# Optimization experiments

Measured on AMD Instinct MI355X. Metric: run time of the kernel, lower is better.

The kernel has to match this reference:

```python
import jax, jax.numpy as jnp
import numpy as np
import math

B, S, H, DK = 16, 4096, 16, 64
DM = H * DK          # 1024, d_model
QD = 1024            # q_d_model
KVD = 1024           # kv_d_model
MASK_P = 0.85        # randbool probability


def setup_inputs() -> dict:
    key = jax.random.key(0)
    ks = jax.random.split(key, 12)
    s = 0.02
    return {
        "q": jax.random.normal(ks[0], (B, 1, QD), jnp.float32),
        "k": jax.random.normal(ks[1], (B, S, KVD), jnp.float32),
        "v": jax.random.normal(ks[2], (B, S, KVD), jnp.float32),
        "Wq": jax.random.normal(ks[3], (QD, DM), jnp.float32) * s,
        "bq": jnp.zeros((DM,), jnp.float32),
        "Wk": jax.random.normal(ks[4], (KVD, DM), jnp.float32) * s,
        "bk": jnp.zeros((DM,), jnp.float32),
        "Wv": jax.random.normal(ks[5], (KVD, DM), jnp.float32) * s,
        "bv": jnp.zeros((DM,), jnp.float32),
        "Wo": jax.random.normal(ks[6], (DM, QD), jnp.float32) * s,
        "bo": jnp.zeros((QD,), jnp.float32),
        # randbool(shape, p=0.85): True where rand < p -> score zeroed
        "maskfill": jax.random.uniform(ks[7], (B, H, 1, S)) < MASK_P,
    }


def reference(q, k, v, Wq, bq, Wk, bk, Wv, bv, Wo, bo, maskfill):
    bs = q.shape[0]
    # projections -> [B, L, H, DK] -> [B, H, L, DK]
    qh = (q @ Wq + bq).reshape(bs, -1, H, DK).transpose(0, 2, 1, 3)  # [B,H,1,DK]
    kh = (k @ Wk + bk).reshape(bs, -1, H, DK).transpose(0, 2, 1, 3)  # [B,H,S,DK]
    vh = (v @ Wv + bv).reshape(bs, -1, H, DK).transpose(0, 2, 1, 3)  # [B,H,S,DK]

    scores1 = jnp.einsum("bhqd,bhkd->bhqk", qh, kh) / math.sqrt(DK)  # [B,H,1,S]

    # plain path (dropout = identity in eval)
    attn = jax.nn.softmax(scores1, axis=-1)
    out_h = jnp.einsum("bhqk,bhkd->bhqd", attn, vh)                  # [B,H,1,DK]

    # masked path: zero-fill (not -inf) masked raw scores, then softmax
    masked_scores = jnp.where(maskfill, 0.0, scores1)
    mattn = jax.nn.softmax(masked_scores, axis=-1)
    mout_h = jnp.einsum("bhqk,bhkd->bhqd", mattn, vh)

    concat = out_h.transpose(0, 2, 1, 3).reshape(bs, DM)
    mconcat = mout_h.transpose(0, 2, 1, 3).reshape(bs, DM)
    output = concat @ Wo + bo
    masked_output = mconcat @ Wo + bo
    return (output, masked_output)
```

## Files before the change

kernel.cpp:

```cpp
#include <hip/hip_runtime.h>
#include <stdint.h>

#define NB 16
#define NS 4096
#define NH 16
#define NC 1024

#define OFF_QHP   0u
#define OFF_QK    262144u
#define OFF_QB    524288u
#define OFF_FLAG  524544u
#define OFF_SP    524608u
#define OFF_S     532800u
#define OFF_ATT   533312u
#define OFF_CTXP  2630464u
#define OFF_CTX   6824768u
#define OFF_CON   7349056u

__global__ void k_maskprobe(const uint32_t* __restrict__ m, int* __restrict__ flag) {
    __shared__ int sf, sg;
    if (threadIdx.x == 0) { sf = 0; sg = 0; }
    __syncthreads();
    uint32_t x = m[threadIdx.x];
    if (x == 0x3F800000u) atomicOr(&sf, 1);
    else if (x > 1u) atomicOr(&sg, 1);
    __syncthreads();
    if (threadIdx.x == 0) *flag = sf ? 2 : (sg ? 1 : 0);
}

__global__ __launch_bounds__(128) void k_qh(
    const float* __restrict__ q, const float* __restrict__ Wq, float* __restrict__ qhp)
{
    __shared__ float qs[64*16];
    int dz = blockIdx.x, cs = blockIdx.y;
    int tid = threadIdx.x;
    int d = dz*128 + tid;
#pragma unroll
    for (int j = 0; j < 2; ++j) {
        int idx = j*128 + tid;
        int b = idx >> 4, c4 = (idx & 15) << 2;
        float4 t = *(const float4*)(q + (size_t)b*NC + cs*64 + c4);
        qs[(c4+0)*16 + b] = t.x; qs[(c4+1)*16 + b] = t.y;
        qs[(c4+2)*16 + b] = t.z; qs[(c4+3)*16 + b] = t.w;
    }
    __syncthreads();
    float acc[16];
#pragma unroll
    for (int b = 0; b < 16; ++b) acc[b] = 0.f;
#pragma unroll 4
    for (int c = 0; c < 64; ++c) {
        float w = Wq[(size_t)(cs*64 + c)*NC + d];
        const float4* qr = (const float4*)(qs + c*16);
        float4 q0 = qr[0], q1 = qr[1], q2 = qr[2], q3 = qr[3];
        acc[0]  = fmaf(w, q0.x, acc[0]);  acc[1]  = fmaf(w, q0.y, acc[1]);
        acc[2]  = fmaf(w, q0.z, acc[2]);  acc[3]  = fmaf(w, q0.w, acc[3]);
        acc[4]  = fmaf(w, q1.x, acc[4]);  acc[5]  = fmaf(w, q1.y, acc[5]);
        acc[6]  = fmaf(w, q1.z, acc[6]);  acc[7]  = fmaf(w, q1.w, acc[7]);
        acc[8]  = fmaf(w, q2.x, acc[8]);  acc[9]  = fmaf(w, q2.y, acc[9]);
        acc[10] = fmaf(w, q2.z, acc[10]); acc[11] = fmaf(w, q2.w, acc[11]);
        acc[12] = fmaf(w, q3.x, acc[12]); acc[13] = fmaf(w, q3.y, acc[13]);
        acc[14] = fmaf(w, q3.z, acc[14]); acc[15] = fmaf(w, q3.w, acc[15]);
    }
#pragma unroll
    for (int b = 0; b < 16; ++b) qhp[((size_t)cs*16 + b)*NC + d] = acc[b];
}

__global__ __launch_bounds__(128) void k_qk(
    const float* __restrict__ qhp, const float* __restrict__ bq,
    const float* __restrict__ Wk, const float* __restrict__ bk,
    float* __restrict__ qko, float* __restrict__ qbv)
{
    int h = blockIdx.x;
    int c = blockIdx.y*128 + threadIdx.x;
    __shared__ float qs[16*64];
    for (int j = 0; j < 8; ++j) {
        int idx = j*128 + threadIdx.x;
        int b = idx >> 6, dd = idx & 63;
        float a = bq[h*64 + dd];
#pragma unroll
        for (int cs = 0; cs < 16; ++cs) a += qhp[((size_t)cs*16 + b)*NC + h*64 + dd];
        qs[idx] = a;
    }
    __syncthreads();
    const float* wr = Wk + (size_t)c*NC + h*64;
    float acc[16];
#pragma unroll
    for (int b = 0; b < 16; ++b) acc[b] = 0.f;
#pragma unroll 4
    for (int d = 0; d < 64; ++d) {
        float w = wr[d];
#pragma unroll
        for (int b = 0; b < 16; ++b) acc[b] = fmaf(qs[b*64 + d], w, acc[b]);
    }
#pragma unroll
    for (int b = 0; b < 16; ++b) qko[((size_t)b*NH + h)*NC + c] = acc[b];
    if (blockIdx.y == 0 && threadIdx.x < 16) {
        int b = threadIdx.x; float a = 0.f;
        for (int d = 0; d < 64; ++d) a = fmaf(qs[b*64 + d], bk[h*64 + d], a);
        qbv[b*NH + h] = a;
    }
}

#define QTS 20
__global__ __launch_bounds__(256) void k_scoresG(
    const float* __restrict__ kk, const float* __restrict__ qkm,
    const float* __restrict__ qbv, const void* __restrict__ mask,
    const int* __restrict__ flagp, float* __restrict__ att, float* __restrict__ Sp)
{
    __shared__ float qt[NC*QTS];
    __shared__ float red[4][32];
    int sb = blockIdx.x, b = blockIdx.y;
    int tid = threadIdx.x;
    for (int idx = tid; idx < NH*NC; idx += 256) {
        int c = idx & 1023, h = idx >> 10;
        qt[c*QTS + h] = qkm[((size_t)b*NH + h)*NC + c];
    }
    __syncthreads();

    int g = tid >> 2, ph = tid & 3;
    int s0 = sb*256;
    const float* kbase = kk + ((size_t)b*NS + s0 + g*4)*NC + ph*4;
    float acc[4][16];
#pragma unroll
    for (int i = 0; i < 4; ++i)
#pragma unroll
        for (int h = 0; h < 16; ++h) acc[i][h] = 0.f;

    float4 kv[4], kn[4];
#pragma unroll
    for (int i = 0; i < 4; ++i) kv[i] = *(const float4*)(kbase + i*NC);
    for (int w = 0; w < 64; ++w) {
        if (w < 63) {
#pragma unroll
            for (int i = 0; i < 4; ++i)
                kn[i] = *(const float4*)(kbase + i*NC + (w+1)*16);
        }
#pragma unroll
        for (int j = 0; j < 4; ++j) {
            int c = w*16 + ph*4 + j;
            const float* qp = qt + c*QTS;
            float4 q0 = *(const float4*)(qp + 0);
            float4 q1 = *(const float4*)(qp + 4);
            float4 q2 = *(const float4*)(qp + 8);
            float4 q3 = *(const float4*)(qp + 12);
#pragma unroll
            for (int i = 0; i < 4; ++i) {
                float kc = (j == 0) ? kv[i].x : (j == 1) ? kv[i].y
                         : (j == 2) ? kv[i].z : kv[i].w;
                acc[i][0]  = fmaf(kc, q0.x, acc[i][0]);
                acc[i][1]  = fmaf(kc, q0.y, acc[i][1]);
                acc[i][2]  = fmaf(kc, q0.z, acc[i][2]);
                acc[i][3]  = fmaf(kc, q0.w, acc[i][3]);
                acc[i][4]  = fmaf(kc, q1.x, acc[i][4]);
                acc[i][5]  = fmaf(kc, q1.y, acc[i][5]);
                acc[i][6]  = fmaf(kc, q1.z, acc[i][6]);
                acc[i][7]  = fmaf(kc, q1.w, acc[i][7]);
                acc[i][8]  = fmaf(kc, q2.x, acc[i][8]);
                acc[i][9]  = fmaf(kc, q2.y, acc[i][9]);
                acc[i][10] = fmaf(kc, q2.z, acc[i][10]);
                acc[i][11] = fmaf(kc, q2.w, acc[i][11]);
                acc[i][12] = fmaf(kc, q3.x, acc[i][12]);
                acc[i][13] = fmaf(kc, q3.y, acc[i][13]);
                acc[i][14] = fmaf(kc, q3.z, acc[i][14]);
                acc[i][15] = fmaf(kc, q3.w, acc[i][15]);
            }
        }
#pragma unroll
        for (int i = 0; i < 4; ++i) kv[i] = kn[i];
    }

#pragma unroll
    for (int i = 0; i < 4; ++i)
#pragma unroll
        for (int h = 0; h < 16; ++h) {
            acc[i][h] += __shfl_xor(acc[i][h], 1, 64);
            acc[i][h] += __shfl_xor(acc[i][h], 2, 64);
        }

    float sc[16];
#pragma unroll
    for (int i = 0; i < 4; ++i)
        if (ph == i) {
#pragma unroll
            for (int h = 0; h < 16; ++h) sc[h] = acc[i][h];
        }

    int s = s0 + tid;
    int fl = *flagp;
    unsigned mbits = 0;
    if (fl == 1) {
        const uint8_t* mp = (const uint8_t*)mask + (size_t)b*NH*NS + s;
#pragma unroll
        for (int h = 0; h < 16; ++h) if (mp[(size_t)h*NS]) mbits |= (1u << h);
    } else if (fl == 2) {
        const float* mp = (const float*)mask + (size_t)b*NH*NS + s;
#pragma unroll
        for (int h = 0; h < 16; ++h) if (mp[(size_t)h*NS] != 0.f) mbits |= (1u << h);
    } else {
        const int* mp = (const int*)mask + (size_t)b*NH*NS + s;
#pragma unroll
        for (int h = 0; h < 16; ++h) if (mp[(size_t)h*NS]) mbits |= (1u << h);
    }

    float p0[16], p1[16];
    float r0[16], r1[16];
#pragma unroll
    for (int h = 0; h < 16; ++h) {
        float val = (sc[h] + qbv[b*NH + h]) * 0.125f;
        p0[h] = __expf(val);
        p1[h] = (mbits >> h & 1u) ? 1.0f : p0[h];
        r0[h] = p0[h]; r1[h] = p1[h];
    }
    float* arow = att + ((size_t)b*NS + s)*32;
    *(float4*)(arow +  0) = make_float4(p0[0],  p0[1],  p0[2],  p0[3]);
    *(float4*)(arow +  4) = make_float4(p0[4],  p0[5],  p0[6],  p0[7]);
    *(float4*)(arow +  8) = make_float4(p0[8],  p0[9],  p0[10], p0[11]);
    *(float4*)(arow + 12) = make_float4(p0[12], p0[13], p0[14], p0[15]);
    *(float4*)(arow + 16) = make_float4(p1[0],  p1[1],  p1[2],  p1[3]);
    *(float4*)(arow + 20) = make_float4(p1[4],  p1[5],  p1[6],  p1[7]);
    *(float4*)(arow + 24) = make_float4(p1[8],  p1[9],  p1[10], p1[11]);
    *(float4*)(arow + 28) = make_float4(p1[12], p1[13], p1[14], p1[15]);

#pragma unroll
    for (int off = 1; off < 64; off <<= 1)
#pragma unroll
        for (int h = 0; h < 16; ++h) {
            r0[h] += __shfl_xor(r0[h], off, 64);
            r1[h] += __shfl_xor(r1[h], off, 64);
        }
    int wv = tid >> 6;
    if ((tid & 63) == 0) {
#pragma unroll
        for (int h = 0; h < 16; ++h) { red[wv][h] = r0[h]; red[wv][16+h] = r1[h]; }
    }
    __syncthreads();
    if (tid < 32)
        Sp[((size_t)b*16 + sb)*32 + tid] =
            red[0][tid] + red[1][tid] + red[2][tid] + red[3][tid];
}

__global__ void k_sred(const float* __restrict__ Sp, float* __restrict__ S) {
    int t = blockIdx.x*256 + threadIdx.x;
    int p = t >> 8, b = (t >> 4) & 15, h = t & 15;
    float a = 0.f;
#pragma unroll
    for (int sb = 0; sb < 16; ++sb) a += Sp[((size_t)b*16 + sb)*32 + p*16 + h];
    S[t] = a;
}

__global__ __launch_bounds__(256,2) void k_ctx(
    const float* __restrict__ v, const float* __restrict__ att, float* __restrict__ ctxp)
{
    __shared__ float al[64*32];
    __shared__ float buf[8192];
    int b = blockIdx.x & 15, ss = blockIdx.x >> 4;
    int cz = blockIdx.y;
    int tid = threadIdx.x, ct = tid & 63, rg = tid >> 6;
    int s1 = ss * 512;
    float acc[32][4];
#pragma unroll
    for (int i = 0; i < 32; ++i)
#pragma unroll
        for (int j = 0; j < 4; ++j) acc[i][j] = 0.f;

    for (int c0 = 0; c0 < 512; c0 += 64) {
        __syncthreads();
#pragma unroll
        for (int jj = 0; jj < 2; ++jj) {
            int idx = jj*256 + tid;
            ((float4*)al)[idx] = ((const float4*)(att + ((size_t)b*NS + s1 + c0)*32))[idx];
        }
        __syncthreads();
        for (int it = 0; it < 16; ++it) {
            int rl = c0 + it*4 + rg;
            float4 vv = *(const float4*)(v + ((size_t)b*NS + s1 + rl)*NC + cz*256 + ct*4);
            const float4* ar = (const float4*)(al + (it*4 + rg)*32);
#pragma unroll
            for (int u = 0; u < 8; ++u) {
                float4 aw = ar[u];
                acc[u*4+0][0] = fmaf(aw.x, vv.x, acc[u*4+0][0]);
                acc[u*4+0][1] = fmaf(aw.x, vv.y, acc[u*4+0][1]);
                acc[u*4+0][2] = fmaf(aw.x, vv.z, acc[u*4+0][2]);
                acc[u*4+0][3] = fmaf(aw.x, vv.w, acc[u*4+0][3]);
                acc[u*4+1][0] = fmaf(aw.y, vv.x, acc[u*4+1][0]);
                acc[u*4+1][1] = fmaf(aw.y, vv.y, acc[u*4+1][1]);
                acc[u*4+1][2] = fmaf(aw.y, vv.z, acc[u*4+1][2]);
                acc[u*4+1][3] = fmaf(aw.y, vv.w, acc[u*4+1][3]);
                acc[u*4+2][0] = fmaf(aw.z, vv.x, acc[u*4+2][0]);
                acc[u*4+2][1] = fmaf(aw.z, vv.y, acc[u*4+2][1]);
                acc[u*4+2][2] = fmaf(aw.z, vv.z, acc[u*4+2][2]);
                acc[u*4+2][3] = fmaf(aw.z, vv.w, acc[u*4+2][3]);
                acc[u*4+3][0] = fmaf(aw.w, vv.x, acc[u*4+3][0]);
                acc[u*4+3][1] = fmaf(aw.w, vv.y, acc[u*4+3][1]);
                acc[u*4+3][2] = fmaf(aw.w, vv.z, acc[u*4+3][2]);
                acc[u*4+3][3] = fmaf(aw.w, vv.w, acc[u*4+3][3]);
            }
        }
    }
    for (int pr = 0; pr < 4; ++pr) {
        __syncthreads();
#pragma unroll
        for (int u = 0; u < 8; ++u) {
            int ph = pr*8 + u;
            float4 t; t.x = acc[ph][0]; t.y = acc[ph][1]; t.z = acc[ph][2]; t.w = acc[ph][3];
            ((float4*)buf)[(rg*8 + u)*64 + ct] = t;
        }
        __syncthreads();
#pragma unroll
        for (int kx = 0; kx < 2; ++kx) {
            int i = kx*256 + tid;
            int u2 = i >> 6, c2 = i & 63;
            float4 s = ((float4*)buf)[(size_t)(0*8 + u2)*64 + c2];
#pragma unroll
            for (int r2 = 1; r2 < 4; ++r2) {
                float4 t = ((float4*)buf)[(size_t)(r2*8 + u2)*64 + c2];
                s.x += t.x; s.y += t.y; s.z += t.z; s.w += t.w;
            }
            int ph = pr*8 + u2, p = ph >> 4, h = ph & 15;
            *(float4*)(ctxp + ((((size_t)ss*2 + p)*NB + b)*NH + h)*NC + cz*256 + c2*4) = s;
        }
    }
}

__global__ void k_ctxred(const float* __restrict__ ctxp, const float* __restrict__ S,
                         float* __restrict__ ctx) {
    size_t i = (size_t)blockIdx.x * 256 + threadIdx.x;
    float a = 0.f;
#pragma unroll
    for (int ss = 0; ss < 8; ++ss) a += ctxp[(size_t)ss*524288 + i];
    ctx[i] = a / S[i >> 10];
}

__global__ __launch_bounds__(256) void k_outh(
    const float* __restrict__ ctx, const float* __restrict__ Wv,
    const float* __restrict__ bv, float* __restrict__ con)
{
    int b = blockIdx.y, p = blockIdx.z;
    int d = blockIdx.x*256 + threadIdx.x;
    int h0 = blockIdx.x*4;
    __shared__ float cl[4*NC];
    for (int i = threadIdx.x; i < 4*NC; i += 256)
        cl[i] = ctx[(((size_t)p*NB + b)*NH + h0 + (i >> 10))*NC + (i & 1023)];
    __syncthreads();
    const float* c2 = cl + ((threadIdx.x >> 6) << 10);
    float a0=0.f,a1=0.f,a2=0.f,a3=0.f;
    for (int c = 0; c < NC; c += 4) {
        a0 = fmaf(c2[c+0], Wv[(size_t)(c+0)*NC + d], a0);
        a1 = fmaf(c2[c+1], Wv[(size_t)(c+1)*NC + d], a1);
        a2 = fmaf(c2[c+2], Wv[(size_t)(c+2)*NC + d], a2);
        a3 = fmaf(c2[c+3], Wv[(size_t)(c+3)*NC + d], a3);
    }
    con[((size_t)p*NB + b)*NC + d] = (a0+a1)+(a2+a3) + bv[d];
}

__global__ __launch_bounds__(256) void k_out(
    const float* __restrict__ con, const float* __restrict__ Wo,
    const float* __restrict__ bo, float* __restrict__ out)
{
    int b = blockIdx.y, p = blockIdx.z;
    int o = blockIdx.x*256 + threadIdx.x;
    __shared__ float cl[NC];
    for (int i = threadIdx.x; i < NC; i += 256)
        cl[i] = con[((size_t)p*NB + b)*NC + i];
    __syncthreads();
    float a0=0.f,a1=0.f,a2=0.f,a3=0.f;
    for (int m = 0; m < NC; m += 4) {
        a0 = fmaf(cl[m+0], Wo[(size_t)(m+0)*NC + o], a0);
        a1 = fmaf(cl[m+1], Wo[(size_t)(m+1)*NC + o], a1);
        a2 = fmaf(cl[m+2], Wo[(size_t)(m+2)*NC + o], a2);
        a3 = fmaf(cl[m+3], Wo[(size_t)(m+3)*NC + o], a3);
    }
    out[(size_t)p*NB*NC + (size_t)b*NC + o] = (a0+a1)+(a2+a3) + bo[o];
}

extern "C" void kernel_launch(void* const* d_in, const int* in_sizes, int n_in,
                              void* d_out, int out_size, void* d_ws, size_t ws_size,
                              hipStream_t stream)
{
    (void)in_sizes; (void)n_in; (void)out_size; (void)ws_size;
    const float* q  = (const float*)d_in[0];
    const float* k  = (const float*)d_in[1];
    const float* v  = (const float*)d_in[2];
    const float* Wq = (const float*)d_in[3];
    const float* bq = (const float*)d_in[4];
    const float* Wk = (const float*)d_in[5];
    const float* bk = (const float*)d_in[6];
    const float* Wv = (const float*)d_in[7];
    const float* bv = (const float*)d_in[8];
    const float* Wo = (const float*)d_in[9];
    const float* bo = (const float*)d_in[10];
    const void*  mk = d_in[11];

    float* ws   = (float*)d_ws;
    float* qhp  = ws + OFF_QHP;
    float* qkv  = ws + OFF_QK;
    float* qbv  = ws + OFF_QB;
    int*   flg  = (int*)(ws + OFF_FLAG);
    float* Sp   = ws + OFF_SP;
    float* S    = ws + OFF_S;
    float* att  = ws + OFF_ATT;
    float* ctxp = ws + OFF_CTXP;
    float* ctx  = ws + OFF_CTX;
    float* con  = ws + OFF_CON;
    float* out  = (float*)d_out;

    k_maskprobe<<<1, 1024, 0, stream>>>((const uint32_t*)mk, flg);
    k_qh<<<dim3(8, 16), 128, 0, stream>>>(q, Wq, qhp);
    k_qk<<<dim3(16, 8), 128, 0, stream>>>(qhp, bq, Wk, bk, qkv, qbv);
    k_scoresG<<<dim3(16, 16), 256, 0, stream>>>(k, qkv, qbv, mk, flg, att, Sp);
    k_sred<<<2, 256, 0, stream>>>(Sp, S);
    k_ctx<<<dim3(128, 4), 256, 0, stream>>>(v, att, ctxp);
    k_ctxred<<<2048, 256, 0, stream>>>(ctxp, S, ctx);
    k_outh<<<dim3(4, NB, 2), 256, 0, stream>>>(ctx, Wv, bv, con);
    k_out<<<dim3(4, NB, 2), 256, 0, stream>>>(con, Wo, bo, out);
}
```

Baseline: 306.4 us.

## Split scores and context kernels across more blocks for higher occupancy

The scores kernel now gives each block 64 sequence rows instead of 256, so each thread owns one row quarter with 16 accumulators rather than 64. The query-key table is staged through shared memory in four 256-channel chunks, which shrinks the LDS footprint. The grid grows from 256 to 1024 blocks, and the context kernel doubles its grid by halving the span each block covers. The aim is to fill the GPU's compute units better on these two memory-bound passes, at the cost of more partial sums to reduce, more workspace and extra barriers.

```diff
diff --git a/kernel.cpp b/kernel.cpp
--- a/kernel.cpp
+++ b/kernel.cpp
@@ -11,11 +11,11 @@
 #define OFF_QB    524288u
 #define OFF_FLAG  524544u
 #define OFF_SP    524608u
-#define OFF_S     532800u
-#define OFF_ATT   533312u
-#define OFF_CTXP  2630464u
-#define OFF_CTX   6824768u
-#define OFF_CON   7349056u
+#define OFF_S     557376u
+#define OFF_ATT   557888u
+#define OFF_CTXP  2655040u
+#define OFF_CTX   11043648u
+#define OFF_CON   11567936u
 
 __global__ void k_maskprobe(const uint32_t* __restrict__ m, int* __restrict__ flag) {
     __shared__ int sf, sg;
@@ -102,141 +102,116 @@
 }
 
 #define QTS 20
-__global__ __launch_bounds__(256) void k_scoresG(
+__global__ __launch_bounds__(256) void k_scoresG2(
     const float* __restrict__ kk, const float* __restrict__ qkm,
     const float* __restrict__ qbv, const void* __restrict__ mask,
     const int* __restrict__ flagp, float* __restrict__ att, float* __restrict__ Sp)
 {
-    __shared__ float qt[NC*QTS];
-    __shared__ float red[4][32];
+    __shared__ float qt[256*QTS];
+    __shared__ float red[4][2][16];
     int sb = blockIdx.x, b = blockIdx.y;
     int tid = threadIdx.x;
-    for (int idx = tid; idx < NH*NC; idx += 256) {
-        int c = idx & 1023, h = idx >> 10;
-        qt[c*QTS + h] = qkm[((size_t)b*NH + h)*NC + c];
-    }
-    __syncthreads();
-
     int g = tid >> 2, ph = tid & 3;
-    int s0 = sb*256;
-    const float* kbase = kk + ((size_t)b*NS + s0 + g*4)*NC + ph*4;
-    float acc[4][16];
-#pragma unroll
-    for (int i = 0; i < 4; ++i)
-#pragma unroll
-        for (int h = 0; h < 16; ++h) acc[i][h] = 0.f;
-
-    float4 kv[4], kn[4];
-#pragma unroll
-    for (int i = 0; i < 4; ++i) kv[i] = *(const float4*)(kbase + i*NC);
-    for (int w = 0; w < 64; ++w) {
-        if (w < 63) {
-#pragma unroll
-            for (int i = 0; i < 4; ++i)
-                kn[i] = *(const float4*)(kbase + i*NC + (w+1)*16);
-        }
-#pragma unroll
-        for (int j = 0; j < 4; ++j) {
-            int c = w*16 + ph*4 + j;
-            const float* qp = qt + c*QTS;
-            float4 q0 = *(const float4*)(qp + 0);
-            float4 q1 = *(const float4*)(qp + 4);
-            float4 q2 = *(const float4*)(qp + 8);
-            float4 q3 = *(const float4*)(qp + 12);
-#pragma unroll
-            for (int i = 0; i < 4; ++i) {
-                float kc = (j == 0) ? kv[i].x : (j == 1) ? kv[i].y
-                         : (j == 2) ? kv[i].z : kv[i].w;
-                acc[i][0]  = fmaf(kc, q0.x, acc[i][0]);
-                acc[i][1]  = fmaf(kc, q0.y, acc[i][1]);
-                acc[i][2]  = fmaf(kc, q0.z, acc[i][2]);
-                acc[i][3]  = fmaf(kc, q0.w, acc[i][3]);
-                acc[i][4]  = fmaf(kc, q1.x, acc[i][4]);
-                acc[i][5]  = fmaf(kc, q1.y, acc[i][5]);
-                acc[i][6]  = fmaf(kc, q1.z, acc[i][6]);
-                acc[i][7]  = fmaf(kc, q1.w, acc[i][7]);
-                acc[i][8]  = fmaf(kc, q2.x, acc[i][8]);
-                acc[i][9]  = fmaf(kc, q2.y, acc[i][9]);
-                acc[i][10] = fmaf(kc, q2.z, acc[i][10]);
-                acc[i][11] = fmaf(kc, q2.w, acc[i][11]);
-                acc[i][12] = fmaf(kc, q3.x, acc[i][12]);
-                acc[i][13] = fmaf(kc, q3.y, acc[i][13]);
-                acc[i][14] = fmaf(kc, q3.z, acc[i][14]);
-                acc[i][15] = fmaf(kc, q3.w, acc[i][15]);
+    int s = sb*64 + g;
+    const float* kbase = kk + ((size_t)b*NS + s)*NC + ph*4;
+    float acc[16];
+#pragma unroll
+    for (int h = 0; h < 16; ++h) acc[h] = 0.f;
+
+    for (int cz = 0; cz < 4; ++cz) {
+        __syncthreads();
+#pragma unroll
+        for (int j = 0; j < 16; ++j) {
+            int idx = j*256 + tid;
+            int h = idx >> 8, c = idx & 255;
+            qt[c*QTS + h] = qkm[((size_t)b*NH + h)*NC + cz*256 + c];
+        }
+        __syncthreads();
+#pragma unroll
+        for (int w = 0; w < 16; ++w) {
+            float4 kv = *(const float4*)(kbase + cz*256 + w*16);
+#pragma unroll
+            for (int j = 0; j < 4; ++j) {
+                float kc = (j == 0) ? kv.x : (j == 1) ? kv.y : (j == 2) ? kv.z : kv.w;
+                const float* qp = qt + (w*16 + ph*4 + j)*QTS;
+                float4 q0 = *(const float4*)(qp + 0);
+                float4 q1 = *(const float4*)(qp + 4);
+                float4 q2 = *(const float4*)(qp + 8);
+                float4 q3 = *(const float4*)(qp + 12);
+                acc[0]  = fmaf(kc, q0.x, acc[0]);
+                acc[1]  = fmaf(kc, q0.y, acc[1]);
+                acc[2]  = fmaf(kc, q0.z, acc[2]);
+                acc[3]  = fmaf(kc, q0.w, acc[3]);
+                acc[4]  = fmaf(kc, q1.x, acc[4]);
+                acc[5]  = fmaf(kc, q1.y, acc[5]);
+                acc[6]  = fmaf(kc, q1.z, acc[6]);
+                acc[7]  = fmaf(kc, q1.w, acc[7]);
+                acc[8]  = fmaf(kc, q2.x, acc[8]);
+                acc[9]  = fmaf(kc, q2.y, acc[9]);
+                acc[10] = fmaf(kc, q2.z, acc[10]);
+                acc[11] = fmaf(kc, q2.w, acc[11]);
+                acc[12] = fmaf(kc, q3.x, acc[12]);
+                acc[13] = fmaf(kc, q3.y, acc[13]);
+                acc[14] = fmaf(kc, q3.z, acc[14]);
+                acc[15] = fmaf(kc, q3.w, acc[15]);
             }
         }
-#pragma unroll
-        for (int i = 0; i < 4; ++i) kv[i] = kn[i];
-    }
-
-#pragma unroll
-    for (int i = 0; i < 4; ++i)
-#pragma unroll
-        for (int h = 0; h < 16; ++h) {
-            acc[i][h] += __shfl_xor(acc[i][h], 1, 64);
-            acc[i][h] += __shfl_xor(acc[i][h], 2, 64);
-        }
-
-    float sc[16];
-#pragma unroll
-    for (int i = 0; i < 4; ++i)
-        if (ph == i) {
-#pragma unroll
-            for (int h = 0; h < 16; ++h) sc[h] = acc[i][h];
-        }
-
-    int s = s0 + tid;
+    }
+#pragma unroll
+    for (int h = 0; h < 16; ++h) {
+        acc[h] += __shfl_xor(acc[h], 1, 64);
+        acc[h] += __shfl_xor(acc[h], 2, 64);
+    }
+
+    int h0 = ph*4;
     int fl = *flagp;
     unsigned mbits = 0;
     if (fl == 1) {
-        const uint8_t* mp = (const uint8_t*)mask + (size_t)b*NH*NS + s;
-#pragma unroll
-        for (int h = 0; h < 16; ++h) if (mp[(size_t)h*NS]) mbits |= (1u << h);
+        const uint8_t* mp = (const uint8_t*)mask + (size_t)(b*NH + h0)*NS + s;
+#pragma unroll
+        for (int j = 0; j < 4; ++j) if (mp[(size_t)j*NS]) mbits |= (1u << j);
     } else if (fl == 2) {
-        const float* mp = (const float*)mask + (size_t)b*NH*NS + s;
-#pragma unroll
-        for (int h = 0; h < 16; ++h) if (mp[(size_t)h*NS] != 0.f) mbits |= (1u << h);
+        const float* mp = (const float*)mask + (size_t)(b*NH + h0)*NS + s;
+#pragma unroll
+        for (int j = 0; j < 4; ++j) if (mp[(size_t)j*NS] != 0.f) mbits |= (1u << j);
     } else {
-        const int* mp = (const int*)mask + (size_t)b*NH*NS + s;
-#pragma unroll
-        for (int h = 0; h < 16; ++h) if (mp[(size_t)h*NS]) mbits |= (1u << h);
-    }
-
-    float p0[16], p1[16];
-    float r0[16], r1[16];
-#pragma unroll
-    for (int h = 0; h < 16; ++h) {
-        float val = (sc[h] + qbv[b*NH + h]) * 0.125f;
-        p0[h] = __expf(val);
-        p1[h] = (mbits >> h & 1u) ? 1.0f : p0[h];
-        r0[h] = p0[h]; r1[h] = p1[h];
+        const int* mp = (const int*)mask + (size_t)(b*NH + h0)*NS + s;
+#pragma unroll
+        for (int j = 0; j < 4; ++j) if (mp[(size_t)j*NS]) mbits |= (1u << j);
+    }
+    float p0[4], p1[4], r0[4], r1[4];
+#pragma unroll
+    for (int j = 0; j < 4; ++j) {
+        float val = (acc[h0+j] + qbv[b*NH + h0 + j]) * 0.125f;
+        p0[j] = __expf(val);
+        p1[j] = (mbits >> j & 1u) ? 1.0f : p0[j];
+        r0[j] = p0[j]; r1[j] = p1[j];
     }
     float* arow = att + ((size_t)b*NS + s)*32;
-    *(float4*)(arow +  0) = make_float4(p0[0],  p0[1],  p0[2],  p0[3]);
-    *(float4*)(arow +  4) = make_float4(p0[4],  p0[5],  p0[6],  p0[7]);
-    *(float4*)(arow +  8) = make_float4(p0[8],  p0[9],  p0[10], p0[11]);
-    *(float4*)(arow + 12) = make_float4(p0[12], p0[13], p0[14], p0[15]);
-    *(float4*)(arow + 16) = make_float4(p1[0],  p1[1],  p1[2],  p1[3]);
-    *(float4*)(arow + 20) = make_float4(p1[4],  p1[5],  p1[6],  p1[7]);
-    *(float4*)(arow + 24) = make_float4(p1[8],  p1[9],  p1[10], p1[11]);
-    *(float4*)(arow + 28) = make_float4(p1[12], p1[13], p1[14], p1[15]);
-
-#pragma unroll
-    for (int off = 1; off < 64; off <<= 1)
-#pragma unroll
-        for (int h = 0; h < 16; ++h) {
-            r0[h] += __shfl_xor(r0[h], off, 64);
-            r1[h] += __shfl_xor(r1[h], off, 64);
+    *(float4*)(arow + h0)      = make_float4(p0[0], p0[1], p0[2], p0[3]);
+    *(float4*)(arow + 16 + h0) = make_float4(p1[0], p1[1], p1[2], p1[3]);
+
+#pragma unroll
+    for (int off = 4; off < 64; off <<= 1)
+#pragma unroll
+        for (int j = 0; j < 4; ++j) {
+            r0[j] += __shfl_xor(r0[j], off, 64);
+            r1[j] += __shfl_xor(r1[j], off, 64);
         }
     int wv = tid >> 6;
-    if ((tid & 63) == 0) {
-#pragma unroll
-        for (int h = 0; h < 16; ++h) { red[wv][h] = r0[h]; red[wv][16+h] = r1[h]; }
-    }
-    __syncthreads();
-    if (tid < 32)
-        Sp[((size_t)b*16 + sb)*32 + tid] =
-            red[0][tid] + red[1][tid] + red[2][tid] + red[3][tid];
+    if ((tid & 63) < 4) {
+#pragma unroll
+        for (int j = 0; j < 4; ++j) {
+            red[wv][0][(tid & 3)*4 + j] = r0[j];
+            red[wv][1][(tid & 3)*4 + j] = r1[j];
+        }
+    }
+    __syncthreads();
+    if (tid < 32) {
+        int pa = tid >> 4, h = tid & 15;
+        Sp[((size_t)b*64 + sb)*32 + tid] =
+            red[0][pa][h] + red[1][pa][h] + red[2][pa][h] + red[3][pa][h];
+    }
 }
 
 __global__ void k_sred(const float* __restrict__ Sp, float* __restrict__ S) {
@@ -244,7 +219,7 @@
     int p = t >> 8, b = (t >> 4) & 15, h = t & 15;
     float a = 0.f;
 #pragma unroll
-    for (int sb = 0; sb < 16; ++sb) a += Sp[((size_t)b*16 + sb)*32 + p*16 + h];
+    for (int sb = 0; sb < 64; ++sb) a += Sp[((size_t)b*64 + sb)*32 + p*16 + h];
     S[t] = a;
 }
 
@@ -256,14 +231,14 @@
     int b = blockIdx.x & 15, ss = blockIdx.x >> 4;
     int cz = blockIdx.y;
     int tid = threadIdx.x, ct = tid & 63, rg = tid >> 6;
-    int s1 = ss * 512;
+    int s1 = ss * 256;
     float acc[32][4];
 #pragma unroll
     for (int i = 0; i < 32; ++i)
 #pragma unroll
         for (int j = 0; j < 4; ++j) acc[i][j] = 0.f;
 
-    for (int c0 = 0; c0 < 512; c0 += 64) {
+    for (int c0 = 0; c0 < 256; c0 += 64) {
         __syncthreads();
 #pragma unroll
         for (int jj = 0; jj < 2; ++jj) {
@@ -327,7 +302,7 @@
     size_t i = (size_t)blockIdx.x * 256 + threadIdx.x;
     float a = 0.f;
 #pragma unroll
-    for (int ss = 0; ss < 8; ++ss) a += ctxp[(size_t)ss*524288 + i];
+    for (int ss = 0; ss < 16; ++ss) a += ctxp[(size_t)ss*524288 + i];
     ctx[i] = a / S[i >> 10];
 }
 
@@ -407,9 +382,9 @@
     k_maskprobe<<<1, 1024, 0, stream>>>((const uint32_t*)mk, flg);
     k_qh<<<dim3(8, 16), 128, 0, stream>>>(q, Wq, qhp);
     k_qk<<<dim3(16, 8), 128, 0, stream>>>(qhp, bq, Wk, bk, qkv, qbv);
-    k_scoresG<<<dim3(16, 16), 256, 0, stream>>>(k, qkv, qbv, mk, flg, att, Sp);
+    k_scoresG2<<<dim3(64, 16), 256, 0, stream>>>(k, qkv, qbv, mk, flg, att, Sp);
     k_sred<<<2, 256, 0, stream>>>(Sp, S);
-    k_ctx<<<dim3(128, 4), 256, 0, stream>>>(v, att, ctxp);
+    k_ctx<<<dim3(256, 4), 256, 0, stream>>>(v, att, ctxp);
     k_ctxred<<<2048, 256, 0, stream>>>(ctxp, S, ctx);
     k_outh<<<dim3(4, NB, 2), 256, 0, stream>>>(ctx, Wv, bv, con);
     k_out<<<dim3(4, NB, 2), 256, 0, stream>>>(con, Wo, bo, out);
```

After: 307.3 us. Within noise of the previous version (+0.3%).
